# Kernel tuning notes

Hardware: AMD Instinct MI355X
Metric: run time of the kernel (lower is better)

## Reference

```python
import jax, jax.numpy as jnp
import numpy as np

GROUPS = 32
EPS = 1e-6


def group_norm(x, gamma, beta):
    b, h, w, c = x.shape
    xg = x.reshape(b, h, w, GROUPS, c // GROUPS)
    mean = jnp.mean(xg, axis=(1, 2, 4), keepdims=True)
    var = jnp.var(xg, axis=(1, 2, 4), keepdims=True)
    xg = (xg - mean) * jax.lax.rsqrt(var + EPS)
    return xg.reshape(b, h, w, c) * gamma + beta


def setup_inputs() -> dict:
    key = jax.random.key(0)
    ks = jax.random.split(key, 6)
    B, H, W, C = 4, 64, 64, 512
    scale = 0.02
    return {
        "x": jax.random.normal(ks[0], (B, H, W, C), dtype=jnp.float32),
        "gamma": jnp.ones((C,), dtype=jnp.float32),
        "beta": jnp.zeros((C,), dtype=jnp.float32),
        "wq": jax.random.normal(ks[1], (C, C), dtype=jnp.float32) * scale,
        "bq": jnp.zeros((C,), dtype=jnp.float32),
        "wk": jax.random.normal(ks[2], (C, C), dtype=jnp.float32) * scale,
        "bk": jnp.zeros((C,), dtype=jnp.float32),
        "wv": jax.random.normal(ks[3], (C, C), dtype=jnp.float32) * scale,
        "bv": jnp.zeros((C,), dtype=jnp.float32),
        "wo": jax.random.normal(ks[4], (C, C), dtype=jnp.float32) * scale,
        "bo": jnp.zeros((C,), dtype=jnp.float32),
    }


def reference(x, gamma, beta, wq, bq, wk, bk, wv, bv, wo, bo):
    b, h, w, c = x.shape
    xn = group_norm(x, gamma, beta)
    # 1x1 convs == per-pixel linear layers
    q = (jnp.einsum('bhwc,cd->bhwd', xn, wq) + bq).reshape(b, h * w, c)
    k = (jnp.einsum('bhwc,cd->bhwd', xn, wk) + bk).reshape(b, h * w, c)
    v = (jnp.einsum('bhwc,cd->bhwd', xn, wv) + bv).reshape(b, h * w, c)
    # full (hw x hw) attention, single head
    scores = jnp.einsum('bic,bjc->bij', q, k) * (c ** -0.5)  # [b, hw, hw]
    attn = jax.nn.softmax(scores, axis=-1)
    out = jnp.einsum('bij,bjc->bic', attn, v).reshape(b, h, w, c)
    return jnp.einsum('bhwc,cd->bhwd', out, wo) + bo + x
```

## Files before the change

### kernel.cpp

```cpp
#include <hip/hip_runtime.h>
#include <stdint.h>


typedef __attribute__((ext_vector_type(8))) short bf16x8;
typedef __attribute__((ext_vector_type(8))) unsigned short u16x8;
typedef __attribute__((ext_vector_type(4))) float f32x4;

#define SOFTMAX_SCALE 0.044194173824159216f
#define QSCALE 0.06376237087058025f

__device__ __forceinline__ unsigned short f2bf(float f) {
  unsigned int x = __float_as_uint(f);
  x += 0x7fffu + ((x >> 16) & 1u);
  return (unsigned short)(x >> 16);
}
__device__ __forceinline__ float bf2f(unsigned short u) {
  return __uint_as_float((unsigned int)u << 16);
}

__device__ __forceinline__ void gl_lds16(const void* g, void* l) {
  __builtin_amdgcn_global_load_lds(
      (__attribute__((address_space(1))) unsigned char*)g,
      (__attribute__((address_space(3))) unsigned char*)l, 16, 0, 0);
}

__device__ __forceinline__ void gemm_tile(
    const unsigned short* __restrict__ A, long lda,
    const unsigned short* __restrict__ B, long ldb,
    int K,
    unsigned short* As0, unsigned short* As1,
    unsigned short* Bs0, unsigned short* Bs1,
    f32x4 acc[4][4]) {
  const int tid = threadIdx.x;
  const int wave = tid >> 6, lane = tid & 63;
  const int srow = lane >> 3;
  const int gg = lane & 7;
  const int wm = (wave >> 1) * 64, wn = (wave & 1) * 64;
  const int lrow = lane & 15;
  const int rsw = lrow & 7;
  const int kgb = lane >> 4;

  auto STAGE = [&](unsigned short* as, unsigned short* bs, int k0) {
#pragma unroll
    for (int i = 0; i < 4; ++i) {
      int chunk = wave * 4 + i;
      int row = chunk * 8 + srow;
      int soffA = (gg ^ srow) * 16;
      int soffB = (gg ^ ((chunk * 2 + (srow >> 2)) & 7)) * 16;
      gl_lds16((const char*)(A + (long)row * lda + k0) + soffA, (char*)as + chunk * 1024);
      gl_lds16((const char*)(B + (long)row * ldb + k0) + soffB, (char*)bs + chunk * 1024);
    }
  };

  auto COMPUTE = [&](const unsigned short* as, const unsigned short* bs) {
#pragma unroll
    for (int ks = 0; ks < 2; ++ks) {
      bf16x8 af[4], bfr[4];
      const int off = ((ks * 4 + kgb) ^ rsw) * 8;
#pragma unroll
      for (int t = 0; t < 4; ++t) {
        af[t]  = *(const bf16x8*)&as[(wm + t * 16 + lrow) * 64 + off];
        bfr[t] = *(const bf16x8*)&bs[(wn + 4 * lrow + t) * 64 + off];
      }
#pragma unroll
      for (int mt = 0; mt < 4; ++mt)
#pragma unroll
        for (int nt = 0; nt < 4; ++nt)
          acc[mt][nt] = __builtin_amdgcn_mfma_f32_16x16x32_bf16(af[mt], bfr[nt], acc[mt][nt], 0, 0, 0);
    }
  };

  const int nk = K >> 6;
  STAGE(As0, Bs0, 0);
  __syncthreads();
  for (int t = 0; t < nk; t += 2) {
    if (t + 1 < nk) STAGE(As1, Bs1, (t + 1) * 64);
    COMPUTE(As0, Bs0);
    __syncthreads();
    if (t + 2 < nk) STAGE(As0, Bs0, (t + 2) * 64);
    COMPUTE(As1, Bs1);
    __syncthreads();
  }
}

#define GEMM_SHARED                                              \
  __shared__ unsigned short As0[128 * 64], As1[128 * 64];        \
  __shared__ unsigned short Bs0[128 * 64], Bs1[128 * 64];

#define EPILOG_SETUP                                          \
  const int lane = threadIdx.x & 63, wave = threadIdx.x >> 6; \
  const int wm = (wave >> 1) * 64, wn = (wave & 1) * 64;      \
  const int lcol4 = (lane & 15) * 4, lrb = (lane >> 4) * 4;

__global__ void prep_kernel(const float* __restrict__ wq, const float* __restrict__ wk,
                            const float* __restrict__ wv, const float* __restrict__ wo,
                            const float* __restrict__ bq, const float* __restrict__ bk,
                            const float* __restrict__ bv,
                            unsigned short* __restrict__ wqkvT,
                            unsigned short* __restrict__ woT,
                            float* __restrict__ bias, float* __restrict__ stats,
                            float* __restrict__ lsum) {
  long id = (long)blockIdx.x * 256 + threadIdx.x;
  if (id < 786432) {
    long n = id >> 9, k = id & 511;
    const float* w = (n < 512) ? wq : (n < 1024 ? wk : wv);
    wqkvT[id] = f2bf(w[k * 512 + (n & 511)]);
  } else if (id < 786432 + 262144) {
    long j = id - 786432, n = j >> 9, k = j & 511;
    woT[j] = f2bf(wo[k * 512 + n]);
  } else if (id < 786432 + 262144 + 1536) {
    long j = id - 786432 - 262144;
    bias[j] = (j < 512) ? bq[j] : (j < 1024 ? bk[j - 512] : bv[j - 1024]);
  } else if (id < 786432 + 262144 + 1536 + 256) {
    stats[id - 786432 - 262144 - 1536] = 0.f;
  } else if (id < 786432 + 262144 + 1536 + 256 + 16384) {
    lsum[id - 786432 - 262144 - 1536 - 256] = 0.f;
  }
}

__global__ __launch_bounds__(256) void gn_stats(const float* __restrict__ x,
                                                float* __restrict__ stats) {
  const int b = blockIdx.x >> 7, slab = blockIdx.x & 127;
  const float* xp = x + (long)b * 4096 * 512 + (long)slab * 32 * 512;
  const int tid = threadIdx.x;
  float s = 0.f, s2 = 0.f;
  for (int it = 0; it < 16; ++it) {
    int i = it * 256 + tid;
    float4 v = *(const float4*)(xp + (long)i * 4);
    s += v.x + v.y + v.z + v.w;
    s2 += v.x * v.x + v.y * v.y + v.z * v.z + v.w * v.w;
  }
  s += __shfl_xor(s, 1); s += __shfl_xor(s, 2);
  s2 += __shfl_xor(s2, 1); s2 += __shfl_xor(s2, 2);
  if ((tid & 3) == 0) {
    int g = (tid & 127) >> 2;
    atomicAdd(&stats[(b * 32 + g) * 2], s);
    atomicAdd(&stats[(b * 32 + g) * 2 + 1], s2);
  }
}

__global__ __launch_bounds__(256) void gn_apply(const float* __restrict__ x,
                                                const float* __restrict__ stats,
                                                const float* __restrict__ gamma,
                                                const float* __restrict__ beta,
                                                unsigned short* __restrict__ xn) {
  long id = (long)blockIdx.x * 256 + threadIdx.x;
  long a = id * 4;
  int b = (int)(id >> 19);
  int ch = (int)(a & 511);
  int g = ch >> 4;
  float s = stats[(b * 32 + g) * 2], s2 = stats[(b * 32 + g) * 2 + 1];
  float mean = s * (1.f / 65536.f);
  float rinv = rsqrtf(s2 * (1.f / 65536.f) - mean * mean + 1e-6f);
  float4 v = *(const float4*)(x + a);
  float4 gm = *(const float4*)(gamma + ch);
  float4 bt = *(const float4*)(beta + ch);
  ushort4 o;
  o.x = f2bf((v.x - mean) * rinv * gm.x + bt.x);
  o.y = f2bf((v.y - mean) * rinv * gm.y + bt.y);
  o.z = f2bf((v.z - mean) * rinv * gm.z + bt.z);
  o.w = f2bf((v.w - mean) * rinv * gm.w + bt.w);
  *(ushort4*)(xn + a) = o;
}

__global__ __launch_bounds__(256) void qkv_kernel(
    const unsigned short* __restrict__ xn, const unsigned short* __restrict__ wqkvT,
    const float* __restrict__ bias, unsigned short* __restrict__ q,
    unsigned short* __restrict__ kk, unsigned short* __restrict__ vv) {
  GEMM_SHARED
  f32x4 acc[4][4] = {};
  const long tm = (long)blockIdx.x * 128, tn = (long)blockIdx.y * 128;
  gemm_tile(xn + tm * 512, 512, wqkvT + tn * 512, 512, 512, As0, As1, Bs0, Bs1, acc);
  EPILOG_SETUP
  const int region = (int)(tn >> 9);
  unsigned short* dst = region == 0 ? q : (region == 1 ? kk : vv);
  const long nloc = (tn & 511) + wn + lcol4;
  const float sc = region == 0 ? QSCALE : 1.f;
  float4 bs = *(const float4*)&bias[tn + wn + lcol4];
#pragma unroll
  for (int mt = 0; mt < 4; ++mt)
#pragma unroll
    for (int r = 0; r < 4; ++r) {
      long m = tm + wm + mt * 16 + lrb + r;
      ushort4 o;
      o.x = f2bf((acc[mt][0][r] + bs.x) * sc);
      o.y = f2bf((acc[mt][1][r] + bs.y) * sc);
      o.z = f2bf((acc[mt][2][r] + bs.z) * sc);
      o.w = f2bf((acc[mt][3][r] + bs.w) * sc);
      *(ushort4*)&dst[m * 512 + nloc] = o;
    }
}

__global__ __launch_bounds__(256) void transpose_v(const unsigned short* __restrict__ v,
                                                   unsigned short* __restrict__ vT) {
  const int b = blockIdx.z;
  const long j0 = (long)blockIdx.x * 64, c0 = (long)blockIdx.y * 64;
  __shared__ unsigned short t[64][72];
  const int tc = (threadIdx.x & 15) * 4, tr = threadIdx.x >> 4;
  for (int rr = 0; rr < 64; rr += 16) {
    ushort4 u = *(const ushort4*)&v[((long)b * 4096 + j0 + tr + rr) * 512 + c0 + tc];
    t[tr + rr][tc] = u.x; t[tr + rr][tc + 1] = u.y;
    t[tr + rr][tc + 2] = u.z; t[tr + rr][tc + 3] = u.w;
  }
  __syncthreads();
  for (int rr = 0; rr < 64; rr += 16) {
    int c = tr + rr;
    ushort4 o;
    o.x = t[tc + 0][c]; o.y = t[tc + 1][c]; o.z = t[tc + 2][c]; o.w = t[tc + 3][c];
    *(ushort4*)&vT[((long)b * 512 + c0 + c) * 4096 + j0 + tc] = o;
  }
}

__global__ __launch_bounds__(256) void qkt_kernel(
    const unsigned short* __restrict__ q, const unsigned short* __restrict__ kk,
    unsigned short* __restrict__ probs, float* __restrict__ lsum, int b0) {
  GEMM_SHARED
  f32x4 acc[4][4] = {};
  const int z = blockIdx.z;
  const long bb = (long)(b0 + z) * 4096 * 512;
  const long tm = (long)blockIdx.x * 128, tn = (long)blockIdx.y * 128;
  gemm_tile(q + bb + tm * 512, 512, kk + bb + tn * 512, 512, 512, As0, As1, Bs0, Bs1, acc);
  EPILOG_SETUP
  unsigned short* out = probs + (long)z * 4096 * 4096;
  float* ls = lsum + (long)(b0 + z) * 4096;
  const long n0 = tn + wn + lcol4;
#pragma unroll
  for (int mt = 0; mt < 4; ++mt) {
    float rs[4];
#pragma unroll
    for (int r = 0; r < 4; ++r) {
      float e0 = exp2f(acc[mt][0][r]);
      float e1 = exp2f(acc[mt][1][r]);
      float e2 = exp2f(acc[mt][2][r]);
      float e3 = exp2f(acc[mt][3][r]);
      rs[r] = (e0 + e1) + (e2 + e3);
      ushort4 o;
      o.x = f2bf(e0); o.y = f2bf(e1); o.z = f2bf(e2); o.w = f2bf(e3);
      long m = tm + wm + mt * 16 + lrb + r;
      *(ushort4*)&out[m * 4096 + n0] = o;
    }
#pragma unroll
    for (int r = 0; r < 4; ++r) {
      float s = rs[r];
      s += __shfl_xor(s, 1); s += __shfl_xor(s, 2);
      s += __shfl_xor(s, 4); s += __shfl_xor(s, 8);
      if (lcol4 == 0) atomicAdd(&ls[tm + wm + mt * 16 + lrb + r], s);
    }
  }
}

__global__ __launch_bounds__(256) void pv_kernel(
    const unsigned short* __restrict__ probs, const unsigned short* __restrict__ vT,
    const float* __restrict__ lsum, unsigned short* __restrict__ attn, int b0) {
  GEMM_SHARED
  f32x4 acc[4][4] = {};
  const int z = blockIdx.z;
  const long tm = (long)blockIdx.x * 128, tn = (long)blockIdx.y * 128;
  gemm_tile(probs + (long)z * 4096 * 4096 + tm * 4096, 4096,
            vT + (long)(b0 + z) * 512 * 4096 + tn * 4096, 4096,
            4096, As0, As1, Bs0, Bs1, acc);
  EPILOG_SETUP
  unsigned short* out = attn + (long)(b0 + z) * 4096 * 512;
  const float* ls = lsum + (long)(b0 + z) * 4096;
  const long n0 = tn + wn + lcol4;
#pragma unroll
  for (int mt = 0; mt < 4; ++mt)
#pragma unroll
    for (int r = 0; r < 4; ++r) {
      long m = tm + wm + mt * 16 + lrb + r;
      float inv = __builtin_amdgcn_rcpf(ls[m]);
      ushort4 o;
      o.x = f2bf(acc[mt][0][r] * inv); o.y = f2bf(acc[mt][1][r] * inv);
      o.z = f2bf(acc[mt][2][r] * inv); o.w = f2bf(acc[mt][3][r] * inv);
      *(ushort4*)&out[m * 512 + n0] = o;
    }
}

__global__ __launch_bounds__(256) void proj_kernel(
    const unsigned short* __restrict__ attn, const unsigned short* __restrict__ woT,
    const float* __restrict__ bo, const float* __restrict__ x,
    float* __restrict__ out) {
  GEMM_SHARED
  f32x4 acc[4][4] = {};
  const long tm = (long)blockIdx.x * 128, tn = (long)blockIdx.y * 128;
  gemm_tile(attn + tm * 512, 512, woT + tn * 512, 512, 512, As0, As1, Bs0, Bs1, acc);
  EPILOG_SETUP
  const long n0 = tn + wn + lcol4;
  float4 bs = *(const float4*)&bo[n0];
#pragma unroll
  for (int mt = 0; mt < 4; ++mt)
#pragma unroll
    for (int r = 0; r < 4; ++r) {
      long m = tm + wm + mt * 16 + lrb + r;
      float4 xv = *(const float4*)&x[m * 512 + n0];
      float4 o;
      o.x = acc[mt][0][r] + bs.x + xv.x;
      o.y = acc[mt][1][r] + bs.y + xv.y;
      o.z = acc[mt][2][r] + bs.z + xv.z;
      o.w = acc[mt][3][r] + bs.w + xv.w;
      *(float4*)&((float*)out)[m * 512 + n0] = o;
    }
}

extern "C" void kernel_launch(void* const* d_in, const int* in_sizes, int n_in,
                              void* d_out, int out_size, void* d_ws, size_t ws_size,
                              hipStream_t stream) {
  const float* x     = (const float*)d_in[0];
  const float* gamma = (const float*)d_in[1];
  const float* beta  = (const float*)d_in[2];
  const float* wq    = (const float*)d_in[3];
  const float* bq    = (const float*)d_in[4];
  const float* wk    = (const float*)d_in[5];
  const float* bk    = (const float*)d_in[6];
  const float* wv    = (const float*)d_in[7];
  const float* bv    = (const float*)d_in[8];
  const float* wo    = (const float*)d_in[9];
  const float* bo    = (const float*)d_in[10];

  char* p = (char*)d_ws;
  auto take = [&](size_t bytes) { char* r = p; p += (bytes + 255) & ~(size_t)255; return r; };
  const long NTOK = 16384, C = 512, HW = 4096;
  unsigned short* xn    = (unsigned short*)take(NTOK * C * 2);
  unsigned short* q     = (unsigned short*)take(NTOK * C * 2);
  unsigned short* kbuf  = (unsigned short*)take(NTOK * C * 2);
  unsigned short* vT    = (unsigned short*)take(NTOK * C * 2);
  unsigned short* wqkvT = (unsigned short*)take(1536l * 512 * 2);
  unsigned short* woT   = (unsigned short*)take(512l * 512 * 2);
  float* bias           = (float*)take(1536 * 4);
  float* stats          = (float*)take(256 * 4);
  float* lsum           = (float*)take(16384 * 4);

  size_t fixed = (size_t)(p - (char*)d_ws);
  size_t per_nb = (size_t)HW * HW * 2 + 512;
  int NB = (ws_size >= fixed + 4 * per_nb) ? 4
         : (ws_size >= fixed + 2 * per_nb) ? 2 : 1;
  unsigned short* probs = (unsigned short*)take((size_t)NB * HW * HW * 2);
  unsigned short* attn  = xn;
  unsigned short* vbuf  = probs;

  prep_kernel<<<4168, 256, 0, stream>>>(wq, wk, wv, wo, bq, bk, bv, wqkvT, woT,
                                        bias, stats, lsum);
  gn_stats<<<512, 256, 0, stream>>>(x, stats);
  gn_apply<<<8192, 256, 0, stream>>>(x, stats, gamma, beta, xn);

  qkv_kernel<<<dim3(128, 12), 256, 0, stream>>>(xn, wqkvT, bias, q, kbuf, vbuf);
  transpose_v<<<dim3(64, 8, 4), 256, 0, stream>>>(vbuf, vT);

  for (int b0 = 0; b0 < 4; b0 += NB) {
    qkt_kernel<<<dim3(32, 32, NB), 256, 0, stream>>>(q, kbuf, probs, lsum, b0);
    pv_kernel<<<dim3(32, 4, NB), 256, 0, stream>>>(probs, vT, lsum, attn, b0);
  }

  proj_kernel<<<dim3(128, 4), 256, 0, stream>>>(attn, woT, bo, x, (float*)d_out);
}
```

Measured before the change: 367.5 us.

## Use 256x256 triple-buffered GEMM tile for QKV and QK^T kernels

Adds a new GEMM tile routine with 256x256 block tiles, 8 waves, a three-stage LDS ring fed by global_load_lds, XOR-swizzled LDS layout and s_setprio around the MFMA bursts. The QKV projection and QK^T score kernels switch to it with 512-thread blocks and fewer workgroups, aiming for more data reuse per LDS load and better overlap of loads with MFMA. The epilogues now write scalar bf16 values with a different lane-to-column mapping instead of ushort4 vectors, which may make stores less coalesced. LDS use per block rises to 96 KB, so occupancy drops.

Result: no change. 372.3 us (+1.3%).

```diff
diff --git a/kernel.cpp b/kernel.cpp
--- a/kernel.cpp
+++ b/kernel.cpp
@@ -6,7 +6,6 @@
 typedef __attribute__((ext_vector_type(8))) unsigned short u16x8;
 typedef __attribute__((ext_vector_type(4))) float f32x4;
 
-#define SOFTMAX_SCALE 0.044194173824159216f
 #define QSCALE 0.06376237087058025f
 
 __device__ __forceinline__ unsigned short f2bf(float f) {
@@ -22,6 +21,81 @@
   __builtin_amdgcn_global_load_lds(
       (__attribute__((address_space(1))) unsigned char*)g,
       (__attribute__((address_space(3))) unsigned char*)l, 16, 0, 0);
+}
+
+__device__ __forceinline__ void gemm256_tile(
+    const unsigned short* __restrict__ A, long lda,
+    const unsigned short* __restrict__ B, long ldb,
+    int NT,
+    unsigned short* lds, f32x4 acc[8][4]) {
+  const int tid = threadIdx.x;
+  const int wave = tid >> 6, lane = tid & 63;
+  const int wm2 = wave >> 2, wn4 = wave & 3;
+  const int lrow = lane & 15, kgb = lane >> 4;
+  const int koff = (kgb ^ ((lrow >> 1) & 3)) * 8;
+  const int srow = tid >> 2;
+  const int sgl = ((tid & 3) ^ ((srow >> 1) & 3)) * 8;
+  const long aoff0 = (long)srow * lda + sgl;
+  const long aoff1 = (long)(srow + 128) * lda + sgl;
+  const long boff0 = (long)srow * ldb + sgl;
+  const long boff1 = (long)(srow + 128) * ldb + sgl;
+  const int ldst = wave * 512;
+
+  auto STAGE_A = [&](int bw, int t) {
+    const unsigned short* s = A + (long)t * 32;
+    unsigned short* d = lds + bw * 16384 + ldst;
+    gl_lds16(s + aoff0, d);
+    gl_lds16(s + aoff1, d + 4096);
+  };
+  auto STAGE_B = [&](int bw, int t) {
+    const unsigned short* s = B + (long)t * 32;
+    unsigned short* d = lds + bw * 16384 + 8192 + ldst;
+    gl_lds16(s + boff0, d);
+    gl_lds16(s + boff1, d + 4096);
+  };
+
+  STAGE_A(0, 0); STAGE_B(0, 0);
+  STAGE_A(1, 1); STAGE_B(1, 1);
+
+  int bb = 0;
+  for (int t = 0; t < NT; ++t) {
+    if (t + 1 < NT) { asm volatile("s_waitcnt vmcnt(4)" ::: "memory"); }
+    else            { asm volatile("s_waitcnt vmcnt(0)" ::: "memory"); }
+    __builtin_amdgcn_s_barrier();
+
+    const unsigned short* aB = lds + bb * 16384 + wm2 * 4096 + lrow * 32 + koff;
+    const unsigned short* bB = lds + bb * 16384 + 8192 + wn4 * 2048 + lrow * 32 + koff;
+    int bw = bb + 2; if (bw >= 3) bw -= 3;
+
+    bf16x8 bf[4], af[4];
+#pragma unroll
+    for (int n = 0; n < 4; ++n) bf[n] = *(const bf16x8*)(bB + n * 512);
+#pragma unroll
+    for (int m = 0; m < 4; ++m) af[m] = *(const bf16x8*)(aB + m * 512);
+    if (t + 2 < NT) STAGE_A(bw, t + 2);
+    __builtin_amdgcn_s_barrier();
+    __builtin_amdgcn_s_setprio(1);
+#pragma unroll
+    for (int m = 0; m < 4; ++m)
+#pragma unroll
+      for (int n = 0; n < 4; ++n)
+        acc[m][n] = __builtin_amdgcn_mfma_f32_16x16x32_bf16(af[m], bf[n], acc[m][n], 0, 0, 0);
+    __builtin_amdgcn_s_setprio(0);
+
+#pragma unroll
+    for (int m = 0; m < 4; ++m) af[m] = *(const bf16x8*)(aB + (4 + m) * 512);
+    if (t + 2 < NT) STAGE_B(bw, t + 2);
+    __builtin_amdgcn_s_barrier();
+    __builtin_amdgcn_s_setprio(1);
+#pragma unroll
+    for (int m = 0; m < 4; ++m)
+#pragma unroll
+      for (int n = 0; n < 4; ++n)
+        acc[4 + m][n] = __builtin_amdgcn_mfma_f32_16x16x32_bf16(af[m], bf[n], acc[4 + m][n], 0, 0, 0);
+    __builtin_amdgcn_s_setprio(0);
+
+    bb = bb + 1; if (bb >= 3) bb = 0;
+  }
 }
 
 __device__ __forceinline__ void gemm_tile(
@@ -163,31 +237,34 @@
   *(ushort4*)(xn + a) = o;
 }
 
-__global__ __launch_bounds__(256) void qkv_kernel(
+__global__ __launch_bounds__(512, 2) void qkv_kernel(
     const unsigned short* __restrict__ xn, const unsigned short* __restrict__ wqkvT,
     const float* __restrict__ bias, unsigned short* __restrict__ q,
     unsigned short* __restrict__ kk, unsigned short* __restrict__ vv) {
-  GEMM_SHARED
-  f32x4 acc[4][4] = {};
-  const long tm = (long)blockIdx.x * 128, tn = (long)blockIdx.y * 128;
-  gemm_tile(xn + tm * 512, 512, wqkvT + tn * 512, 512, 512, As0, As1, Bs0, Bs1, acc);
-  EPILOG_SETUP
+  __shared__ unsigned short lds[49152];
+  f32x4 acc[8][4] = {};
+  const long tm = (long)blockIdx.x * 256, tn = (long)blockIdx.y * 256;
+  gemm256_tile(xn + tm * 512, 512, wqkvT + tn * 512, 512, 16, lds, acc);
+  const int lane = threadIdx.x & 63, wave = threadIdx.x >> 6;
+  const int wm2 = wave >> 2, wn4 = wave & 3;
+  const int lcol = lane & 15, lrb = (lane >> 4) * 4;
   const int region = (int)(tn >> 9);
   unsigned short* dst = region == 0 ? q : (region == 1 ? kk : vv);
-  const long nloc = (tn & 511) + wn + lcol4;
   const float sc = region == 0 ? QSCALE : 1.f;
-  float4 bs = *(const float4*)&bias[tn + wn + lcol4];
-#pragma unroll
-  for (int mt = 0; mt < 4; ++mt)
-#pragma unroll
-    for (int r = 0; r < 4; ++r) {
-      long m = tm + wm + mt * 16 + lrb + r;
-      ushort4 o;
-      o.x = f2bf((acc[mt][0][r] + bs.x) * sc);
-      o.y = f2bf((acc[mt][1][r] + bs.y) * sc);
-      o.z = f2bf((acc[mt][2][r] + bs.z) * sc);
-      o.w = f2bf((acc[mt][3][r] + bs.w) * sc);
-      *(ushort4*)&dst[m * 512 + nloc] = o;
+  float bv[4];
+#pragma unroll
+  for (int nf = 0; nf < 4; ++nf) bv[nf] = bias[tn + wn4 * 64 + nf * 16 + lcol];
+#pragma unroll
+  for (int mf = 0; mf < 8; ++mf)
+#pragma unroll
+    for (int nf = 0; nf < 4; ++nf) {
+      long n = tn + wn4 * 64 + nf * 16 + lcol;
+      long nloc = n & 511;
+#pragma unroll
+      for (int r = 0; r < 4; ++r) {
+        long m = tm + wm2 * 128 + mf * 16 + lrb + r;
+        dst[m * 512 + nloc] = f2bf((acc[mf][nf][r] + bv[nf]) * sc);
+      }
     }
 }
 
@@ -211,40 +288,40 @@
   }
 }
 
-__global__ __launch_bounds__(256) void qkt_kernel(
+__global__ __launch_bounds__(512, 2) void qkt_kernel(
     const unsigned short* __restrict__ q, const unsigned short* __restrict__ kk,
     unsigned short* __restrict__ probs, float* __restrict__ lsum, int b0) {
-  GEMM_SHARED
-  f32x4 acc[4][4] = {};
+  __shared__ unsigned short lds[49152];
+  f32x4 acc[8][4] = {};
   const int z = blockIdx.z;
   const long bb = (long)(b0 + z) * 4096 * 512;
-  const long tm = (long)blockIdx.x * 128, tn = (long)blockIdx.y * 128;
-  gemm_tile(q + bb + tm * 512, 512, kk + bb + tn * 512, 512, 512, As0, As1, Bs0, Bs1, acc);
-  EPILOG_SETUP
+  const long tm = (long)blockIdx.x * 256, tn = (long)blockIdx.y * 256;
+  gemm256_tile(q + bb + tm * 512, 512, kk + bb + tn * 512, 512, 16, lds, acc);
+  const int lane = threadIdx.x & 63, wave = threadIdx.x >> 6;
+  const int wm2 = wave >> 2, wn4 = wave & 3;
+  const int lcol = lane & 15, lrb = (lane >> 4) * 4;
   unsigned short* out = probs + (long)z * 4096 * 4096;
   float* ls = lsum + (long)(b0 + z) * 4096;
-  const long n0 = tn + wn + lcol4;
-#pragma unroll
-  for (int mt = 0; mt < 4; ++mt) {
-    float rs[4];
-#pragma unroll
-    for (int r = 0; r < 4; ++r) {
-      float e0 = exp2f(acc[mt][0][r]);
-      float e1 = exp2f(acc[mt][1][r]);
-      float e2 = exp2f(acc[mt][2][r]);
-      float e3 = exp2f(acc[mt][3][r]);
-      rs[r] = (e0 + e1) + (e2 + e3);
-      ushort4 o;
-      o.x = f2bf(e0); o.y = f2bf(e1); o.z = f2bf(e2); o.w = f2bf(e3);
-      long m = tm + wm + mt * 16 + lrb + r;
-      *(ushort4*)&out[m * 4096 + n0] = o;
+#pragma unroll
+  for (int mf = 0; mf < 8; ++mf) {
+    float rs[4] = {0.f, 0.f, 0.f, 0.f};
+#pragma unroll
+    for (int nf = 0; nf < 4; ++nf) {
+      long n = tn + wn4 * 64 + nf * 16 + lcol;
+#pragma unroll
+      for (int r = 0; r < 4; ++r) {
+        long m = tm + wm2 * 128 + mf * 16 + lrb + r;
+        float e = exp2f(acc[mf][nf][r]);
+        out[m * 4096 + n] = f2bf(e);
+        rs[r] += e;
+      }
     }
 #pragma unroll
     for (int r = 0; r < 4; ++r) {
       float s = rs[r];
       s += __shfl_xor(s, 1); s += __shfl_xor(s, 2);
       s += __shfl_xor(s, 4); s += __shfl_xor(s, 8);
-      if (lcol4 == 0) atomicAdd(&ls[tm + wm + mt * 16 + lrb + r], s);
+      if (lcol == 0) atomicAdd(&ls[tm + wm2 * 128 + mf * 16 + lrb + r], s);
     }
   }
 }
@@ -343,11 +420,11 @@
   gn_stats<<<512, 256, 0, stream>>>(x, stats);
   gn_apply<<<8192, 256, 0, stream>>>(x, stats, gamma, beta, xn);
 
-  qkv_kernel<<<dim3(128, 12), 256, 0, stream>>>(xn, wqkvT, bias, q, kbuf, vbuf);
+  qkv_kernel<<<dim3(64, 6), 512, 0, stream>>>(xn, wqkvT, bias, q, kbuf, vbuf);
   transpose_v<<<dim3(64, 8, 4), 256, 0, stream>>>(vbuf, vT);
 
   for (int b0 = 0; b0 < 4; b0 += NB) {
-    qkt_kernel<<<dim3(32, 32, NB), 256, 0, stream>>>(q, kbuf, probs, lsum, b0);
+    qkt_kernel<<<dim3(16, 16, NB), 512, 0, stream>>>(q, kbuf, probs, lsum, b0);
     pv_kernel<<<dim3(32, 4, NB), 256, 0, stream>>>(probs, vT, lsum, attn, b0);
   }
 
```
